# Performance work log

Measured on AMD Instinct MI355X. Metric: run time of the kernel, lower is better.

The kernel has to match this reference:

```python
import jax, jax.numpy as jnp
import numpy as np

N, D = 4096, 128  # seq length / feature dim of x is N; head dim is D

def setup_inputs() -> dict:
    key = jax.random.key(0)
    k1, k2 = jax.random.split(key)
    x = jax.random.normal(k1, (N, N), dtype=jnp.float32)
    # nn.Linear(N, 3*d): weight [3d, N], bias [3d]; scale weight like torch init
    W = jax.random.normal(k2, (3 * D, N), dtype=jnp.float32) / jnp.sqrt(jnp.float32(N))
    b = jnp.zeros((3 * D,), dtype=jnp.float32)
    return {"x": x, "W": W, "b": b}

def reference(x, W, b):
    # QKV projection: [N, 3d]
    qkv = x @ W.T + b
    Q, K, V = jnp.split(qkv, 3, axis=-1)  # each [N, d]
    # The blockwise online-softmax double loop computes exactly
    # softmax(Q K^T) V with NO 1/sqrt(d) scaling (faithful to source).
    S = Q @ K.T                 # [N, N]
    P = jax.nn.softmax(S, axis=-1)
    return P @ V                # [N, d]
```

## Files before the change

### kernel.cpp

```cpp
#include <hip/hip_runtime.h>
#include <cstdint>
#include <cstddef>

typedef _Float16 f16;
typedef f16 f16x8 __attribute__((ext_vector_type(8)));
typedef f16 f16x4 __attribute__((ext_vector_type(4)));
typedef float f32x4 __attribute__((ext_vector_type(4)));

#define SEQ 4096
#define DH 128
#define QKV_LD 384
#define LOG2E 1.44269504f

__device__ __forceinline__ float fast_exp2(float x) {
#if __has_builtin(__builtin_amdgcn_exp2f)
  return __builtin_amdgcn_exp2f(x);
#else
  return exp2f(x);
#endif
}

__device__ __forceinline__ void gl_lds16(const void* g, void* l) {
  __builtin_amdgcn_global_load_lds((const __attribute__((address_space(1))) void*)g,
                                   (__attribute__((address_space(3))) void*)l, 16, 0, 0);
}

__global__ __launch_bounds__(256) void cvt_w_kernel(const float4* __restrict__ W,
                                                    f16x4* __restrict__ Wh) {
  int i = blockIdx.x * 256 + threadIdx.x;
  float4 v = W[i];
  f16x4 h; h[0] = (f16)v.x; h[1] = (f16)v.y; h[2] = (f16)v.z; h[3] = (f16)v.w;
  Wh[i] = h;
}

template <int SPLITS>
__global__ __launch_bounds__(256, 2) void gemm_qkv(const float* __restrict__ x,
                                                   const f16* __restrict__ Wh,
                                                   f16* __restrict__ part) {
  __shared__ __align__(16) f16 Ax[64][72];
  __shared__ __align__(16) f16 Bx[QKV_LD * 64];
  const int m0 = blockIdx.x * 64;
  const int split = blockIdx.y;
  const int kc = SEQ / SPLITS;
  const int k0 = split * kc;
  const int tid = threadIdx.x;
  const int lane = tid & 63;
  const int wave = tid >> 6;
  const int nb = wave * 96;
  const int l15 = lane & 15, quad = lane >> 4;

  f32x4 acc[4][6] = {};

  for (int kt = k0; kt < k0 + kc; kt += 64) {
#pragma unroll
    for (int r = 0; r < 12; ++r) {
      int c = r * 256 + tid;
      int row = c >> 3, ch = c & 7;
      const f16* src = &Wh[(size_t)row * SEQ + kt + ((ch ^ (row & 7)) << 3)];
      gl_lds16(src, &Bx[(size_t)c << 3]);
    }
#pragma unroll
    for (int r = 0; r < 4; ++r) {
      int c = r * 256 + tid;
      int row = c >> 4, col = (c & 15) * 4;
      float4 v = *(const float4*)&x[(size_t)(m0 + row) * SEQ + kt + col];
      f16x4 h; h[0] = (f16)v.x; h[1] = (f16)v.y; h[2] = (f16)v.z; h[3] = (f16)v.w;
      *(f16x4*)&Ax[row][col] = h;
    }
    __syncthreads();
#pragma unroll
    for (int ks = 0; ks < 2; ++ks) {
      f16x8 a[4], bb[6];
#pragma unroll
      for (int t = 0; t < 4; ++t)
        a[t] = *(const f16x8*)&Ax[t * 16 + l15][ks * 32 + quad * 8];
#pragma unroll
      for (int t = 0; t < 6; ++t) {
        int n = nb + t * 16 + l15;
        int ch = (ks * 4 + quad) ^ (l15 & 7);
        bb[t] = *(const f16x8*)&Bx[((size_t)n << 6) + (ch << 3)];
      }
#pragma unroll
      for (int mt = 0; mt < 4; ++mt)
#pragma unroll
        for (int nt = 0; nt < 6; ++nt)
          acc[mt][nt] = __builtin_amdgcn_mfma_f32_16x16x32_f16(a[mt], bb[nt], acc[mt][nt], 0, 0, 0);
    }
    __syncthreads();
  }

  f16* pw = part + (size_t)split * SEQ * QKV_LD;
#pragma unroll
  for (int mt = 0; mt < 4; ++mt) {
#pragma unroll
    for (int nt = 0; nt < 6; ++nt) {
      int col = nb + nt * 16 + l15;
      int rowbase = m0 + mt * 16 + quad * 4;
#pragma unroll
      for (int rr = 0; rr < 4; ++rr)
        pw[(size_t)(rowbase + rr) * QKV_LD + col] = (f16)acc[mt][nt][rr];
    }
  }
}

template <int SPLITS>
__global__ __launch_bounds__(256) void reduce_qkv(const f16* __restrict__ part,
                                                  const float* __restrict__ bias,
                                                  f16* __restrict__ qkv) {
  int i = (blockIdx.x * 256 + threadIdx.x) * 8;
  float acc[8] = {};
#pragma unroll
  for (int s = 0; s < SPLITS; ++s) {
    f16x8 p = *(const f16x8*)&part[(size_t)s * SEQ * QKV_LD + i];
#pragma unroll
    for (int j = 0; j < 8; ++j) acc[j] += (float)p[j];
  }
  int col = i % QKV_LD;
  f16x8 o;
#pragma unroll
  for (int j = 0; j < 8; ++j) o[j] = (f16)(acc[j] + bias[col + j]);
  *(f16x8*)&qkv[i] = o;
}

__global__ __launch_bounds__(256) void transpose_v(const f16* __restrict__ qkv,
                                                   f16* __restrict__ Vt) {
  __shared__ __align__(16) f16 T[64][72];
  const int r0 = blockIdx.x * 64;
  const int c0 = blockIdx.y * 64;
  const int tid = threadIdx.x;
#pragma unroll
  for (int rep = 0; rep < 2; ++rep) {
    int idx = rep * 256 + tid;
    int row = idx >> 3, col = (idx & 7) * 8;
    *(f16x8*)&T[row][col] = *(const f16x8*)&qkv[(size_t)(r0 + row) * QKV_LD + 256 + c0 + col];
  }
  __syncthreads();
#pragma unroll
  for (int rep = 0; rep < 2; ++rep) {
    int idx = rep * 256 + tid;
    int cc = idx >> 3, rb = (idx & 7) * 8;
    f16x8 o;
#pragma unroll
    for (int j = 0; j < 8; ++j) o[j] = T[rb + j][cc];
    *(f16x8*)&Vt[(size_t)(c0 + cc) * SEQ + r0 + rb] = o;
  }
}

#define NSPLIT 16
#define KVRANGE (SEQ / NSPLIT)

__global__ __launch_bounds__(256, 2) void attn_partial(const f16* __restrict__ qkv,
                                                       const f16* __restrict__ Vt,
                                                       f16* __restrict__ Op,
                                                       float* __restrict__ ml) {
  __shared__ __align__(16) f16 Ks[64][136];
  __shared__ __align__(16) f16 Vs[128][72];
  __shared__ __align__(16) f16 Ps[4][32][72];

  const int q0 = blockIdx.x * 128;
  const int split = blockIdx.y;
  const int kv0 = split * KVRANGE;
  const int tid = threadIdx.x;
  const int lane = tid & 63, wave = tid >> 6;
  const int l15 = lane & 15, quad = lane >> 4;
  const int mbase = q0 + wave * 32;

  f16x8 qf[2][4];
#pragma unroll
  for (int mt = 0; mt < 2; ++mt)
#pragma unroll
    for (int ks = 0; ks < 4; ++ks) {
      f16x8 q = *(const f16x8*)&qkv[(size_t)(mbase + mt * 16 + l15) * QKV_LD + ks * 32 + quad * 8];
      qf[mt][ks] = q * (f16)LOG2E;
    }

  f32x4 oacc[2][8] = {};
  float mrow[2] = {-1e30f, -1e30f};
  float lrow[2] = {0.f, 0.f};

  for (int it = 0; it < KVRANGE / 64; ++it) {
    const int k0 = kv0 + it * 64;
#pragma unroll
    for (int r = 0; r < 4; ++r) {
      int c = tid + r * 256;
      int row = c >> 4, col = (c & 15) * 8;
      *(f16x8*)&Ks[row][col] = *(const f16x8*)&qkv[(size_t)(k0 + row) * QKV_LD + DH + col];
    }
#pragma unroll
    for (int r = 0; r < 4; ++r) {
      int c = tid + r * 256;
      int row = c >> 3, col = (c & 7) * 8;
      *(f16x8*)&Vs[row][col] = *(const f16x8*)&Vt[(size_t)row * SEQ + k0 + col];
    }
    __syncthreads();

    f32x4 st[4][2] = {};
#pragma unroll
    for (int ks = 0; ks < 4; ++ks) {
      f16x8 kf[4];
#pragma unroll
      for (int kt = 0; kt < 4; ++kt)
        kf[kt] = *(const f16x8*)&Ks[kt * 16 + l15][ks * 32 + quad * 8];
#pragma unroll
      for (int kt = 0; kt < 4; ++kt)
#pragma unroll
        for (int mt = 0; mt < 2; ++mt)
          st[kt][mt] = __builtin_amdgcn_mfma_f32_16x16x32_f16(kf[kt], qf[mt][ks], st[kt][mt], 0, 0, 0);
    }

    float al[2];
#pragma unroll
    for (int mt = 0; mt < 2; ++mt) {
      float v = -1e30f;
#pragma unroll
      for (int kt = 0; kt < 4; ++kt)
#pragma unroll
        for (int rr = 0; rr < 4; ++rr) v = fmaxf(v, st[kt][mt][rr]);
      v = fmaxf(v, __shfl_xor(v, 16));
      v = fmaxf(v, __shfl_xor(v, 32));
      float mnew = fmaxf(mrow[mt], v);
      al[mt] = fast_exp2(mrow[mt] - mnew);
      mrow[mt] = mnew;
      float ls = 0.f;
#pragma unroll
      for (int kt = 0; kt < 4; ++kt) {
        f16x4 pk;
#pragma unroll
        for (int rr = 0; rr < 4; ++rr) {
          float p = fast_exp2(st[kt][mt][rr] - mnew);
          ls += p;
          pk[rr] = (f16)p;
        }
        *(f16x4*)&Ps[wave][mt * 16 + l15][kt * 16 + quad * 4] = pk;
      }
      ls += __shfl_xor(ls, 16);
      ls += __shfl_xor(ls, 32);
      lrow[mt] = lrow[mt] * al[mt] + ls;
    }

    float alr[2][4];
#pragma unroll
    for (int mt = 0; mt < 2; ++mt)
#pragma unroll
      for (int rr = 0; rr < 4; ++rr)
        alr[mt][rr] = __shfl(al[mt], quad * 4 + rr);
#pragma unroll
    for (int mt = 0; mt < 2; ++mt)
#pragma unroll
      for (int dt = 0; dt < 8; ++dt)
#pragma unroll
        for (int rr = 0; rr < 4; ++rr)
          oacc[mt][dt][rr] *= alr[mt][rr];

#pragma unroll
    for (int kk = 0; kk < 2; ++kk) {
      f16x8 pf[2];
#pragma unroll
      for (int mt = 0; mt < 2; ++mt)
        pf[mt] = *(const f16x8*)&Ps[wave][mt * 16 + l15][kk * 32 + quad * 8];
#pragma unroll
      for (int dt = 0; dt < 8; ++dt) {
        f16x8 vf = *(const f16x8*)&Vs[dt * 16 + l15][kk * 32 + quad * 8];
#pragma unroll
        for (int mt = 0; mt < 2; ++mt)
          oacc[mt][dt] = __builtin_amdgcn_mfma_f32_16x16x32_f16(pf[mt], vf, oacc[mt][dt], 0, 0, 0);
      }
    }
    __syncthreads();
  }

#pragma unroll
  for (int mt = 0; mt < 2; ++mt)
#pragma unroll
    for (int dt = 0; dt < 8; ++dt)
#pragma unroll
      for (int rr = 0; rr < 4; ++rr) {
        int row = mbase + mt * 16 + quad * 4 + rr;
        Op[((size_t)split * SEQ + row) * DH + dt * 16 + l15] = (f16)oacc[mt][dt][rr];
      }
  if (quad == 0) {
#pragma unroll
    for (int mt = 0; mt < 2; ++mt) {
      int row = mbase + mt * 16 + l15;
      ml[((size_t)split * SEQ + row) * 2 + 0] = mrow[mt];
      ml[((size_t)split * SEQ + row) * 2 + 1] = lrow[mt];
    }
  }
}

__global__ __launch_bounds__(256) void combine_kernel(const f16* __restrict__ Op,
                                                      const float* __restrict__ ml,
                                                      float* __restrict__ out) {
  int idx = blockIdx.x * 256 + threadIdx.x;
  int row = idx >> 7;
  float ms[NSPLIT], ls[NSPLIT];
  float M = -1e30f;
#pragma unroll
  for (int s = 0; s < NSPLIT; ++s) {
    ms[s] = ml[((size_t)s * SEQ + row) * 2 + 0];
    ls[s] = ml[((size_t)s * SEQ + row) * 2 + 1];
    M = fmaxf(M, ms[s]);
  }
  float L = 0.f, o = 0.f;
#pragma unroll
  for (int s = 0; s < NSPLIT; ++s) {
    float w = fast_exp2(ms[s] - M);
    L += ls[s] * w;
    o += w * (float)Op[(size_t)s * SEQ * DH + idx];
  }
  out[idx] = o / L;
}

extern "C" void kernel_launch(void* const* d_in, const int* in_sizes, int n_in,
                              void* d_out, int out_size, void* d_ws, size_t ws_size,
                              hipStream_t stream) {
  const float* x = (const float*)d_in[0];
  const float* W = (const float*)d_in[1];
  const float* b = (const float*)d_in[2];
  float* out = (float*)d_out;
  char* ws = (char*)d_ws;

  f16*   Wh   = (f16*)(ws);
  f16*   qkv  = (f16*)(ws + (3u << 20));
  f16*   Vt   = (f16*)(ws + (6u << 20));
  float* ml   = (float*)(ws + (7u << 20));
  char*  scr  = ws + (7u << 20) + (1u << 19);
  f16*   part = (f16*)scr;
  f16*   Op   = (f16*)scr;

  cvt_w_kernel<<<(384 * 4096 / 4) / 256, 256, 0, stream>>>((const float4*)W, (f16x4*)Wh);

  bool big = ws_size >= ((size_t)31u << 20) + ((size_t)1u << 19);
  if (big) {
    gemm_qkv<8><<<dim3(SEQ / 64, 8), 256, 0, stream>>>(x, Wh, part);
    reduce_qkv<8><<<SEQ * QKV_LD / 8 / 256, 256, 0, stream>>>(part, b, qkv);
  } else {
    gemm_qkv<4><<<dim3(SEQ / 64, 4), 256, 0, stream>>>(x, Wh, part);
    reduce_qkv<4><<<SEQ * QKV_LD / 8 / 256, 256, 0, stream>>>(part, b, qkv);
  }
  transpose_v<<<dim3(SEQ / 64, DH / 64), 256, 0, stream>>>(qkv, Vt);
  attn_partial<<<dim3(SEQ / 128, NSPLIT), 256, 0, stream>>>(qkv, Vt, Op, ml);
  combine_kernel<<<(SEQ * DH) / 256, 256, 0, stream>>>(Op, ml, out);
}
```

Before: 152.0 us.

## Prefetch GEMM and attention tiles into registers, defer softmax rescaling, vectorize reduce/combine

The QKV GEMM and the attention loop now prefetch the next tile's global data into registers while the current tile is being computed. The GEMM partials are written in a fragment-native layout so the reduce kernel can read them contiguously. The attention softmax skips the running-max update and output rescale unless some row's max grows by more than a threshold (lazy rescaling), which saves exp and multiply work. The combine kernel handles 8 elements per thread with vectorized loads and stores. The price is extra register pressure, plus some risk of fp16 overflow in P when the max is stale by up to 2^4.

```diff
diff --git a/kernel.cpp b/kernel.cpp
--- a/kernel.cpp
+++ b/kernel.cpp
@@ -11,6 +11,7 @@
 #define DH 128
 #define QKV_LD 384
 #define LOG2E 1.44269504f
+#define DEFER_THR 4.0f
 
 __device__ __forceinline__ float fast_exp2(float x) {
 #if __has_builtin(__builtin_amdgcn_exp2f)
@@ -50,6 +51,18 @@
   const int l15 = lane & 15, quad = lane >> 4;
 
   f32x4 acc[4][6] = {};
+  float4 areg[4];
+
+#define LOAD_A(KT)                                                         \
+  do {                                                                     \
+    _Pragma("unroll") for (int r = 0; r < 4; ++r) {                        \
+      int c = r * 256 + tid;                                               \
+      int row = c >> 4, col = (c & 15) * 4;                                \
+      areg[r] = *(const float4*)&x[(size_t)(m0 + row) * SEQ + (KT) + col]; \
+    }                                                                      \
+  } while (0)
+
+  LOAD_A(k0);
 
   for (int kt = k0; kt < k0 + kc; kt += 64) {
 #pragma unroll
@@ -63,11 +76,12 @@
     for (int r = 0; r < 4; ++r) {
       int c = r * 256 + tid;
       int row = c >> 4, col = (c & 15) * 4;
-      float4 v = *(const float4*)&x[(size_t)(m0 + row) * SEQ + kt + col];
-      f16x4 h; h[0] = (f16)v.x; h[1] = (f16)v.y; h[2] = (f16)v.z; h[3] = (f16)v.w;
+      f16x4 h; h[0] = (f16)areg[r].x; h[1] = (f16)areg[r].y;
+      h[2] = (f16)areg[r].z; h[3] = (f16)areg[r].w;
       *(f16x4*)&Ax[row][col] = h;
     }
     __syncthreads();
+    if (kt + 64 < k0 + kc) LOAD_A(kt + 64);
 #pragma unroll
     for (int ks = 0; ks < 2; ++ks) {
       f16x8 a[4], bb[6];
@@ -88,17 +102,18 @@
     }
     __syncthreads();
   }
-
-  f16* pw = part + (size_t)split * SEQ * QKV_LD;
+#undef LOAD_A
+
+  f16* pw = part + (((size_t)split * 64 + blockIdx.x) * 24) * 256 * 4;
 #pragma unroll
   for (int mt = 0; mt < 4; ++mt) {
 #pragma unroll
     for (int nt = 0; nt < 6; ++nt) {
-      int col = nb + nt * 16 + l15;
-      int rowbase = m0 + mt * 16 + quad * 4;
-#pragma unroll
-      for (int rr = 0; rr < 4; ++rr)
-        pw[(size_t)(rowbase + rr) * QKV_LD + col] = (f16)acc[mt][nt][rr];
+      int p = mt * 6 + nt;
+      f16x4 h;
+#pragma unroll
+      for (int rr = 0; rr < 4; ++rr) h[rr] = (f16)acc[mt][nt][rr];
+      *(f16x4*)&pw[((size_t)p * 256 + tid) * 4] = h;
     }
   }
 }
@@ -107,19 +122,28 @@
 __global__ __launch_bounds__(256) void reduce_qkv(const f16* __restrict__ part,
                                                   const float* __restrict__ bias,
                                                   f16* __restrict__ qkv) {
-  int i = (blockIdx.x * 256 + threadIdx.x) * 8;
-  float acc[8] = {};
-#pragma unroll
-  for (int s = 0; s < SPLITS; ++s) {
-    f16x8 p = *(const f16x8*)&part[(size_t)s * SEQ * QKV_LD + i];
-#pragma unroll
-    for (int j = 0; j < 8; ++j) acc[j] += (float)p[j];
-  }
-  int col = i % QKV_LD;
-  f16x8 o;
-#pragma unroll
-  for (int j = 0; j < 8; ++j) o[j] = (f16)(acc[j] + bias[col + j]);
-  *(f16x8*)&qkv[i] = o;
+  const int bx = blockIdx.x;
+  const int mt = blockIdx.y;
+  const int tid = threadIdx.x;
+  const int lane = tid & 63, wave = tid >> 6;
+  const int l15 = lane & 15, quad = lane >> 4;
+  const int rowbase = bx * 64 + mt * 16 + quad * 4;
+#pragma unroll
+  for (int nt = 0; nt < 6; ++nt) {
+    const int p = mt * 6 + nt;
+    float acc[4] = {0.f, 0.f, 0.f, 0.f};
+#pragma unroll
+    for (int s = 0; s < SPLITS; ++s) {
+      f16x4 v = *(const f16x4*)&part[((((size_t)s * 64 + bx) * 24 + p) * 256 + tid) * 4];
+#pragma unroll
+      for (int rr = 0; rr < 4; ++rr) acc[rr] += (float)v[rr];
+    }
+    int col = wave * 96 + nt * 16 + l15;
+    float bv = bias[col];
+#pragma unroll
+    for (int rr = 0; rr < 4; ++rr)
+      qkv[(size_t)(rowbase + rr) * QKV_LD + col] = (f16)(acc[rr] + bv);
+  }
 }
 
 __global__ __launch_bounds__(256) void transpose_v(const f16* __restrict__ qkv,
@@ -178,21 +202,38 @@
   float mrow[2] = {-1e30f, -1e30f};
   float lrow[2] = {0.f, 0.f};
 
+  f16x8 kreg[4], vreg[4];
+#define LOAD_TILE(K0)                                                                  \
+  do {                                                                                 \
+    _Pragma("unroll") for (int r = 0; r < 4; ++r) {                                    \
+      int c = tid + r * 256;                                                           \
+      int row = c >> 4, col = (c & 15) * 8;                                            \
+      kreg[r] = *(const f16x8*)&qkv[(size_t)((K0) + row) * QKV_LD + DH + col];         \
+    }                                                                                  \
+    _Pragma("unroll") for (int r = 0; r < 4; ++r) {                                    \
+      int c = tid + r * 256;                                                           \
+      int row = c >> 3, col = (c & 7) * 8;                                             \
+      vreg[r] = *(const f16x8*)&Vt[(size_t)row * SEQ + (K0) + col];                    \
+    }                                                                                  \
+  } while (0)
+
+  LOAD_TILE(kv0);
+
   for (int it = 0; it < KVRANGE / 64; ++it) {
-    const int k0 = kv0 + it * 64;
 #pragma unroll
     for (int r = 0; r < 4; ++r) {
       int c = tid + r * 256;
       int row = c >> 4, col = (c & 15) * 8;
-      *(f16x8*)&Ks[row][col] = *(const f16x8*)&qkv[(size_t)(k0 + row) * QKV_LD + DH + col];
+      *(f16x8*)&Ks[row][col] = kreg[r];
     }
 #pragma unroll
     for (int r = 0; r < 4; ++r) {
       int c = tid + r * 256;
       int row = c >> 3, col = (c & 7) * 8;
-      *(f16x8*)&Vs[row][col] = *(const f16x8*)&Vt[(size_t)row * SEQ + k0 + col];
+      *(f16x8*)&Vs[row][col] = vreg[r];
     }
     __syncthreads();
+    if (it + 1 < KVRANGE / 64) { int k0n = kv0 + (it + 1) * 64; LOAD_TILE(k0n); }
 
     f32x4 st[4][2] = {};
 #pragma unroll
@@ -208,7 +249,7 @@
           st[kt][mt] = __builtin_amdgcn_mfma_f32_16x16x32_f16(kf[kt], qf[mt][ks], st[kt][mt], 0, 0, 0);
     }
 
-    float al[2];
+    float vmax[2];
 #pragma unroll
     for (int mt = 0; mt < 2; ++mt) {
       float v = -1e30f;
@@ -218,16 +259,41 @@
         for (int rr = 0; rr < 4; ++rr) v = fmaxf(v, st[kt][mt][rr]);
       v = fmaxf(v, __shfl_xor(v, 16));
       v = fmaxf(v, __shfl_xor(v, 32));
-      float mnew = fmaxf(mrow[mt], v);
-      al[mt] = fast_exp2(mrow[mt] - mnew);
-      mrow[mt] = mnew;
+      vmax[mt] = v;
+    }
+    bool ok = (vmax[0] <= mrow[0] + DEFER_THR) & (vmax[1] <= mrow[1] + DEFER_THR);
+    if (!__all(ok)) {
+      float al[2];
+#pragma unroll
+      for (int mt = 0; mt < 2; ++mt) {
+        float mnew = fmaxf(mrow[mt], vmax[mt]);
+        al[mt] = fast_exp2(mrow[mt] - mnew);
+        mrow[mt] = mnew;
+        lrow[mt] *= al[mt];
+      }
+      float alr[2][4];
+#pragma unroll
+      for (int mt = 0; mt < 2; ++mt)
+#pragma unroll
+        for (int rr = 0; rr < 4; ++rr)
+          alr[mt][rr] = __shfl(al[mt], quad * 4 + rr);
+#pragma unroll
+      for (int mt = 0; mt < 2; ++mt)
+#pragma unroll
+        for (int dt = 0; dt < 8; ++dt)
+#pragma unroll
+          for (int rr = 0; rr < 4; ++rr)
+            oacc[mt][dt][rr] *= alr[mt][rr];
+    }
+#pragma unroll
+    for (int mt = 0; mt < 2; ++mt) {
       float ls = 0.f;
 #pragma unroll
       for (int kt = 0; kt < 4; ++kt) {
         f16x4 pk;
 #pragma unroll
         for (int rr = 0; rr < 4; ++rr) {
-          float p = fast_exp2(st[kt][mt][rr] - mnew);
+          float p = fast_exp2(st[kt][mt][rr] - mrow[mt]);
           ls += p;
           pk[rr] = (f16)p;
         }
@@ -235,22 +301,8 @@
       }
       ls += __shfl_xor(ls, 16);
       ls += __shfl_xor(ls, 32);
-      lrow[mt] = lrow[mt] * al[mt] + ls;
-    }
-
-    float alr[2][4];
-#pragma unroll
-    for (int mt = 0; mt < 2; ++mt)
-#pragma unroll
-      for (int rr = 0; rr < 4; ++rr)
-        alr[mt][rr] = __shfl(al[mt], quad * 4 + rr);
-#pragma unroll
-    for (int mt = 0; mt < 2; ++mt)
-#pragma unroll
-      for (int dt = 0; dt < 8; ++dt)
-#pragma unroll
-        for (int rr = 0; rr < 4; ++rr)
-          oacc[mt][dt][rr] *= alr[mt][rr];
+      lrow[mt] += ls;
+    }
 
 #pragma unroll
     for (int kk = 0; kk < 2; ++kk) {
@@ -268,6 +320,7 @@
     }
     __syncthreads();
   }
+#undef LOAD_TILE
 
 #pragma unroll
   for (int mt = 0; mt < 2; ++mt)
@@ -291,24 +344,33 @@
 __global__ __launch_bounds__(256) void combine_kernel(const f16* __restrict__ Op,
                                                       const float* __restrict__ ml,
                                                       float* __restrict__ out) {
-  int idx = blockIdx.x * 256 + threadIdx.x;
-  int row = idx >> 7;
+  int t = blockIdx.x * 256 + threadIdx.x;
+  int base = t * 8;
+  int row = base >> 7;
   float ms[NSPLIT], ls[NSPLIT];
   float M = -1e30f;
 #pragma unroll
   for (int s = 0; s < NSPLIT; ++s) {
-    ms[s] = ml[((size_t)s * SEQ + row) * 2 + 0];
-    ls[s] = ml[((size_t)s * SEQ + row) * 2 + 1];
-    M = fmaxf(M, ms[s]);
-  }
-  float L = 0.f, o = 0.f;
+    float2 v = *(const float2*)&ml[((size_t)s * SEQ + row) * 2];
+    ms[s] = v.x; ls[s] = v.y;
+    M = fmaxf(M, v.x);
+  }
+  float L = 0.f;
+  float o[8] = {};
 #pragma unroll
   for (int s = 0; s < NSPLIT; ++s) {
     float w = fast_exp2(ms[s] - M);
     L += ls[s] * w;
-    o += w * (float)Op[(size_t)s * SEQ * DH + idx];
-  }
-  out[idx] = o / L;
+    f16x8 v = *(const f16x8*)&Op[(size_t)s * SEQ * DH + base];
+#pragma unroll
+    for (int j = 0; j < 8; ++j) o[j] += w * (float)v[j];
+  }
+  float inv = 1.0f / L;
+  float4 o0, o1;
+  o0.x = o[0] * inv; o0.y = o[1] * inv; o0.z = o[2] * inv; o0.w = o[3] * inv;
+  o1.x = o[4] * inv; o1.y = o[5] * inv; o1.z = o[6] * inv; o1.w = o[7] * inv;
+  *(float4*)&out[base] = o0;
+  *(float4*)&out[base + 4] = o1;
 }
 
 extern "C" void kernel_launch(void* const* d_in, const int* in_sizes, int n_in,
@@ -333,12 +395,12 @@
   bool big = ws_size >= ((size_t)31u << 20) + ((size_t)1u << 19);
   if (big) {
     gemm_qkv<8><<<dim3(SEQ / 64, 8), 256, 0, stream>>>(x, Wh, part);
-    reduce_qkv<8><<<SEQ * QKV_LD / 8 / 256, 256, 0, stream>>>(part, b, qkv);
+    reduce_qkv<8><<<dim3(64, 4), 256, 0, stream>>>(part, b, qkv);
   } else {
     gemm_qkv<4><<<dim3(SEQ / 64, 4), 256, 0, stream>>>(x, Wh, part);
-    reduce_qkv<4><<<SEQ * QKV_LD / 8 / 256, 256, 0, stream>>>(part, b, qkv);
+    reduce_qkv<4><<<dim3(64, 4), 256, 0, stream>>>(part, b, qkv);
   }
   transpose_v<<<dim3(SEQ / 64, DH / 64), 256, 0, stream>>>(qkv, Vt);
   attn_partial<<<dim3(SEQ / 128, NSPLIT), 256, 0, stream>>>(qkv, Vt, Op, ml);
-  combine_kernel<<<(SEQ * DH) / 256, 256, 0, stream>>>(Op, ml, out);
-}
+  combine_kernel<<<(SEQ * DH) / 8 / 256, 256, 0, stream>>>(Op, ml, out);
+}
```

After: 147.2 us. 3.1% less time.
